# Kernel optimization log

Measured on AMD Instinct MI355X. Metric: run time of the kernel, lower is better.

## Reference

```python
import jax, jax.numpy as jnp
import numpy as np

B, HQ, S, D = 2, 16, 2048, 64   # batch, query heads, seq len, head dim
DV = 2 * D                      # value head dim (differential attention)
LAMBDA_INIT = 0.8
EPS = 1e-5
NEG = -1.0e9


def setup_inputs() -> dict:
    key = jax.random.key(0)
    ks = jax.random.split(key, 8)
    return {
        "q": jax.random.normal(ks[0], (B, HQ, S, D), dtype=jnp.float32),
        "k": jax.random.normal(ks[1], (B, HQ, S, D), dtype=jnp.float32),
        "v": jax.random.normal(ks[2], (B, HQ // 2, S, DV), dtype=jnp.float32),
        "lambda_q1": jax.random.normal(ks[3], (D,), dtype=jnp.float32) * 0.1,
        "lambda_k1": jax.random.normal(ks[4], (D,), dtype=jnp.float32) * 0.1,
        "lambda_q2": jax.random.normal(ks[5], (D,), dtype=jnp.float32) * 0.1,
        "lambda_k2": jax.random.normal(ks[6], (D,), dtype=jnp.float32) * 0.1,
        "gn_weight": jnp.ones((HQ * D,), dtype=jnp.float32),
        "gn_bias": jnp.zeros((HQ * D,), dtype=jnp.float32),
    }


def ghostmax(scores):
    # softmax with an implicit extra zero logit per row
    m = jnp.maximum(jnp.max(scores, axis=-1, keepdims=True), 0.0)
    e = jnp.exp(scores - m)
    return e / (jnp.sum(e, axis=-1, keepdims=True) + jnp.exp(-m))


def group_norm(x, weight, bias, num_groups, eps):
    # x: [B, C, S]; normalize each group over (C/G, S) like nn.GroupNorm
    b, c, s = x.shape
    xg = x.reshape(b, num_groups, (c // num_groups) * s)
    mean = jnp.mean(xg, axis=-1, keepdims=True)
    var = jnp.var(xg, axis=-1, keepdims=True)
    xn = ((xg - mean) * jax.lax.rsqrt(var + eps)).reshape(b, c, s)
    return xn * weight[None, :, None] + bias[None, :, None]


def reference(q, k, v, lambda_q1, lambda_k1, lambda_q2, lambda_k2, gn_weight, gn_bias):
    scale = 1.0 / np.sqrt(D).astype(np.float32)
    scores = jnp.einsum("bhqd,bhkd->bhqk", q, k) * scale
    causal = jnp.triu(jnp.full((S, S), NEG, dtype=scores.dtype), k=1)
    scores = scores + causal[None, None]
    w = ghostmax(scores)                                   # [B, HQ, S, S]
    w = w.reshape(B, HQ // 2, 2, S, S)
    lam1 = jnp.exp(jnp.sum(lambda_q1 * lambda_k1))
    lam2 = jnp.exp(jnp.sum(lambda_q2 * lambda_k2))
    lam = lam1 - lam2 + LAMBDA_INIT
    w = w[:, :, 0] - lam * w[:, :, 1]                      # [B, HQ/2, S, S]
    out = jnp.einsum("bhqk,bhkd->bhqd", w, v)              # [B, HQ/2, S, DV]
    out = out.reshape(B, HQ * D, S)                        # faithful to torch reshape
    out = group_norm(out, gn_weight, gn_bias, num_groups=HQ, eps=EPS)
    return out * (1.0 - LAMBDA_INIT)
```

## Files before the change

kernel.cpp:

```cpp
#include <hip/hip_runtime.h>
#include <hip/hip_bf16.h>

constexpr int B_ = 2, HQ_ = 16, HP_ = 8, S_ = 2048, D_ = 64, DV_ = 128;
constexpr float LAMB0 = 0.8f;
constexpr float EPSV = 1e-5f;

constexpr int TQ = 64, TK = 32;
constexpr int KSTR = 72;
constexpr int VSTR = 40;

typedef __attribute__((ext_vector_type(8))) short bf16x8;
typedef __attribute__((ext_vector_type(4))) float f32x4;
typedef __attribute__((ext_vector_type(8))) float f32x8;

__device__ __forceinline__ unsigned short f2bf(float x) {
  __hip_bfloat16 h = __float2bfloat16(x);
  unsigned short u;
  __builtin_memcpy(&u, &h, 2);
  return u;
}
__device__ __forceinline__ float bf2f(unsigned short h) {
  return __uint_as_float((unsigned)h << 16);
}
__device__ __forceinline__ unsigned pack2(unsigned short a, unsigned short b) {
  return (unsigned)a | ((unsigned)b << 16);
}
__device__ __forceinline__ void split8v(f32x8 x, bf16x8& hi, bf16x8& lo) {
  union { bf16x8 v; unsigned short s[8]; } H, L;
#pragma unroll
  for (int j = 0; j < 8; ++j) {
    unsigned short h = f2bf(x[j]);
    H.s[j] = h;
    L.s[j] = f2bf(x[j] - bf2f(h));
  }
  hi = H.v;
  lo = L.v;
}

__launch_bounds__(512, 4)
__global__ void diffattn_fwd(const float* __restrict__ qg, const float* __restrict__ kg,
                             const float* __restrict__ vg,
                             const float* __restrict__ lq1, const float* __restrict__ lk1,
                             const float* __restrict__ lq2, const float* __restrict__ lk2,
                             float* __restrict__ Obuf, float* __restrict__ stats) {
  __shared__ __align__(16) char smem[38912];
  auto Kl = reinterpret_cast<short(*)[2][TK][KSTR]>(smem);
  auto Vt = reinterpret_cast<short(*)[DV_][VSTR]>(smem + 18432);
  float* mbuf = reinterpret_cast<float*>(smem);
  __shared__ float redbuf[8];

  const int tid = threadIdx.x;
  const int w = tid >> 6;
  const int hw = w >> 2;
  const int qs = w & 3;
  const int l = tid & 63;
  const int g = l >> 4;
  const int li = l & 15;

  const int t = blockIdx.x;
  const int bh = t & 15;
  const int b = bh >> 3;
  const int hp = bh & 7;
  const int u = t >> 4;
  const int qt = (u & 1) ? (31 - (u >> 1)) : (u >> 1);
  const int q0 = qt * TQ;
  const int qw = q0 + qs * 16;

  float d1 = 0.f, d2 = 0.f;
  for (int i = 0; i < D_; ++i) { d1 += lq1[i] * lk1[i]; d2 += lq2[i] * lk2[i]; }
  const float lam = __expf(d1) - __expf(d2) + LAMB0;

  bf16x8 qhi[2], qlo[2];
#pragma unroll
  for (int c = 0; c < 2; ++c) {
    const float* p = qg + (((size_t)b * HQ_ + 2 * hp + hw) * S_ + qw + li) * D_ + c * 32 + g * 8;
    f32x8 x = *reinterpret_cast<const f32x8*>(p);
    split8v(x, qhi[c], qlo[c]);
  }

  float mreg = 0.f;
  float lreg = 1.f;
  const f32x4 zero4 = {0.f, 0.f, 0.f, 0.f};
  f32x4 Oacc[8];
#pragma unroll
  for (int d = 0; d < 8; ++d) Oacc[d] = zero4;

  const int khs = tid >> 8;
  const int kidx = tid & 255;
  const int krow = kidx >> 3;
  const int kcol8 = (kidx & 7) * 8;
  const float* kb0 = kg + ((size_t)b * HQ_ + 2 * hp + khs) * S_ * D_;
  const int vdv = tid & 127;
  const int vk8 = (tid >> 7) * 8;
  const float* vb0 = vg + ((size_t)b * HP_ + hp) * S_ * DV_ + vdv;
  const int vswz = ((vdv >> 3) & 3) << 3;

  const int nkt = (q0 + TQ) / TK;

  for (int kt = 0; kt < nkt; ++kt) {
    const int k0 = kt * TK;
    __syncthreads();

    {
      f32x8 kx = *reinterpret_cast<const f32x8*>(kb0 + (size_t)(k0 + krow) * D_ + kcol8);
      const float* vb = vb0 + (size_t)k0 * DV_;
      f32x8 vx;
#pragma unroll
      for (int j = 0; j < 8; ++j) vx[j] = vb[(size_t)(vk8 + j) * DV_];
      bf16x8 hi, lo;
      split8v(kx, hi, lo);
      *reinterpret_cast<bf16x8*>(&Kl[khs][0][krow][kcol8]) = hi;
      *reinterpret_cast<bf16x8*>(&Kl[khs][1][krow][kcol8]) = lo;
      split8v(vx, hi, lo);
      *reinterpret_cast<bf16x8*>(&Vt[0][vdv][vk8 ^ vswz]) = hi;
      *reinterpret_cast<bf16x8*>(&Vt[1][vdv][vk8 ^ vswz]) = lo;
    }
    __syncthreads();

    if (k0 > qw + 15) continue;
    const bool needmask = (k0 + TK - 1 > qw);
    const int qglob = qw + li;

    bf16x8 kf[2][2][2];
#pragma unroll
    for (int hl = 0; hl < 2; ++hl)
#pragma unroll
      for (int ms = 0; ms < 2; ++ms)
#pragma unroll
        for (int c = 0; c < 2; ++c)
          kf[hl][ms][c] =
              *reinterpret_cast<const bf16x8*>(&Kl[hw][hl][ms * 16 + li][c * 32 + g * 8]);

    f32x4 sT[2] = {zero4, zero4};
    __builtin_amdgcn_s_setprio(1);
#pragma unroll
    for (int ms = 0; ms < 2; ++ms)
#pragma unroll
      for (int c = 0; c < 2; ++c) {
        sT[ms] = __builtin_amdgcn_mfma_f32_16x16x32_bf16(kf[0][ms][c], qhi[c], sT[ms], 0, 0, 0);
        sT[ms] = __builtin_amdgcn_mfma_f32_16x16x32_bf16(kf[0][ms][c], qlo[c], sT[ms], 0, 0, 0);
        sT[ms] = __builtin_amdgcn_mfma_f32_16x16x32_bf16(kf[1][ms][c], qhi[c], sT[ms], 0, 0, 0);
      }
    __builtin_amdgcn_s_setprio(0);

    float sv[2][4];
#pragma unroll
    for (int ms = 0; ms < 2; ++ms)
#pragma unroll
      for (int r = 0; r < 4; ++r) {
        float v = sT[ms][r] * 0.125f;
        if (needmask && (k0 + ms * 16 + g * 4 + r > qglob)) v = -1e30f;
        sv[ms][r] = v;
      }
    float tmax = fmaxf(fmaxf(fmaxf(sv[0][0], sv[0][1]), fmaxf(sv[0][2], sv[0][3])),
                       fmaxf(fmaxf(sv[1][0], sv[1][1]), fmaxf(sv[1][2], sv[1][3])));
    tmax = fmaxf(tmax, __shfl_xor(tmax, 16));
    tmax = fmaxf(tmax, __shfl_xor(tmax, 32));

    if (__any(tmax > mreg + 8.f)) {
      const float mnew = fmaxf(mreg, tmax);
      const float fh = __expf(mreg - mnew);
      mreg = mnew;
      lreg *= fh;
      float fr[4];
#pragma unroll
      for (int r = 0; r < 4; ++r) fr[r] = __shfl(fh, 20 * g + r);
#pragma unroll
      for (int d = 0; d < 8; ++d) {
        f32x4 o = Oacc[d];
        o[0] *= fr[0]; o[1] *= fr[1]; o[2] *= fr[2]; o[3] *= fr[3];
        Oacc[d] = o;
      }
    }

    float p[2][4], psum = 0.f;
#pragma unroll
    for (int ms = 0; ms < 2; ++ms)
#pragma unroll
      for (int r = 0; r < 4; ++r) {
        p[ms][r] = __expf(sv[ms][r] - mreg);
        psum += p[ms][r];
      }
    psum += __shfl_xor(psum, 16);
    psum += __shfl_xor(psum, 32);
    lreg += psum;

    unsigned ph0a = pack2(f2bf(p[0][0]), f2bf(p[0][1]));
    unsigned ph0b = pack2(f2bf(p[0][2]), f2bf(p[0][3]));
    unsigned ph1a = pack2(f2bf(p[1][0]), f2bf(p[1][1]));
    unsigned ph1b = pack2(f2bf(p[1][2]), f2bf(p[1][3]));
    float pl[2][4];
#pragma unroll
    for (int ms = 0; ms < 2; ++ms)
#pragma unroll
      for (int r = 0; r < 4; ++r) pl[ms][r] = p[ms][r] - bf2f(f2bf(p[ms][r]));
    unsigned pl0a = pack2(f2bf(pl[0][0]), f2bf(pl[0][1]));
    unsigned pl0b = pack2(f2bf(pl[0][2]), f2bf(pl[0][3]));
    unsigned pl1a = pack2(f2bf(pl[1][0]), f2bf(pl[1][1]));
    unsigned pl1b = pack2(f2bf(pl[1][2]), f2bf(pl[1][3]));

    const int srcA = 32 * (g & 1) + li;
    const int srcB = srcA + 16;
    const bool hiMs = (g >> 1) != 0;
    bf16x8 AH, AL;
    {
      union { bf16x8 v; unsigned us[4]; } U;
      unsigned a0 = (unsigned)__shfl((int)ph0a, srcA), b0 = (unsigned)__shfl((int)ph1a, srcA);
      unsigned a1 = (unsigned)__shfl((int)ph0b, srcA), b1 = (unsigned)__shfl((int)ph1b, srcA);
      unsigned a2 = (unsigned)__shfl((int)ph0a, srcB), b2 = (unsigned)__shfl((int)ph1a, srcB);
      unsigned a3 = (unsigned)__shfl((int)ph0b, srcB), b3 = (unsigned)__shfl((int)ph1b, srcB);
      U.us[0] = hiMs ? b0 : a0; U.us[1] = hiMs ? b1 : a1;
      U.us[2] = hiMs ? b2 : a2; U.us[3] = hiMs ? b3 : a3;
      AH = U.v;
    }
    {
      union { bf16x8 v; unsigned us[4]; } U;
      unsigned a0 = (unsigned)__shfl((int)pl0a, srcA), b0 = (unsigned)__shfl((int)pl1a, srcA);
      unsigned a1 = (unsigned)__shfl((int)pl0b, srcA), b1 = (unsigned)__shfl((int)pl1b, srcA);
      unsigned a2 = (unsigned)__shfl((int)pl0a, srcB), b2 = (unsigned)__shfl((int)pl1a, srcB);
      unsigned a3 = (unsigned)__shfl((int)pl0b, srcB), b3 = (unsigned)__shfl((int)pl1b, srcB);
      U.us[0] = hiMs ? b0 : a0; U.us[1] = hiMs ? b1 : a1;
      U.us[2] = hiMs ? b2 : a2; U.us[3] = hiMs ? b3 : a3;
      AL = U.v;
    }

    __builtin_amdgcn_s_setprio(1);
#pragma unroll
    for (int dvt = 0; dvt < 8; ++dvt) {
      const int dvr = dvt * 16 + li;
      const int vcol = (g * 8) ^ (((dvr >> 3) & 3) << 3);
      bf16x8 vh = *reinterpret_cast<const bf16x8*>(&Vt[0][dvr][vcol]);
      bf16x8 vl = *reinterpret_cast<const bf16x8*>(&Vt[1][dvr][vcol]);
      f32x4 acc = Oacc[dvt];
      acc = __builtin_amdgcn_mfma_f32_16x16x32_bf16(AH, vh, acc, 0, 0, 0);
      acc = __builtin_amdgcn_mfma_f32_16x16x32_bf16(AL, vh, acc, 0, 0, 0);
      acc = __builtin_amdgcn_mfma_f32_16x16x32_bf16(AH, vl, acc, 0, 0, 0);
      Oacc[dvt] = acc;
    }
    __builtin_amdgcn_s_setprio(0);
  }

  __syncthreads();
  if (w >= 4) {
    float rl[4];
#pragma unroll
    for (int r = 0; r < 4; ++r) rl[r] = lam / __shfl(lreg, 20 * g + r);
#pragma unroll
    for (int dvt = 0; dvt < 8; ++dvt)
#pragma unroll
      for (int r = 0; r < 4; ++r)
        mbuf[((qs * 32 + dvt * 4 + r) * 64) + l] = Oacc[dvt][r] * rl[r];
  }
  __syncthreads();

  float lsum = 0.f, lss = 0.f;
  if (w < 4) {
    float rl[4];
#pragma unroll
    for (int r = 0; r < 4; ++r) rl[r] = 1.f / __shfl(lreg, 20 * g + r);
    float* ob = Obuf + ((size_t)(b * HP_ + hp)) * S_ * DV_;
#pragma unroll
    for (int dvt = 0; dvt < 8; ++dvt)
#pragma unroll
      for (int r = 0; r < 4; ++r) {
        float vres = Oacc[dvt][r] * rl[r] - mbuf[((qs * 32 + dvt * 4 + r) * 64) + l];
        ob[(size_t)(qw + g * 4 + r) * DV_ + dvt * 16 + li] = vres;
        lsum += vres;
        lss += vres * vres;
      }
#pragma unroll
    for (int o = 1; o < 64; o <<= 1) {
      lsum += __shfl_xor(lsum, o);
      lss += __shfl_xor(lss, o);
    }
    if (l == 0) {
      redbuf[w * 2] = lsum;
      redbuf[w * 2 + 1] = lss;
    }
  }
  __syncthreads();
  if (tid == 0) {
    const int region = ((b * HP_ + hp) << 1) | (q0 >= 1024 ? 1 : 0);
    atomicAdd(&stats[2 * region + 0], redbuf[0] + redbuf[2] + redbuf[4] + redbuf[6]);
    atomicAdd(&stats[2 * region + 1], redbuf[1] + redbuf[3] + redbuf[5] + redbuf[7]);
  }
}

__global__ void gn_apply(const float* __restrict__ O, const float* __restrict__ stats,
                         const float* __restrict__ gw, const float* __restrict__ gb,
                         float* __restrict__ out) {
  const size_t f = ((size_t)blockIdx.x * 256 + threadIdx.x) * 4;
  const int g = (int)(f >> 17);
  const int sidx = (int)((f >> 7) & 2047);
  const int hp = (int)((f >> 18) & 7);
  const int c = hp * 128 + (sidx >> 4);
  const float mean = stats[2 * g + 0] * (1.f / 131072.f);
  const float var = stats[2 * g + 1] * (1.f / 131072.f) - mean * mean;
  const float sc = rsqrtf(var + EPSV) * gw[c] * 0.2f;
  const float bi = gb[c] * 0.2f;
  float4 x = *reinterpret_cast<const float4*>(O + f);
  float4 y;
  y.x = (x.x - mean) * sc + bi;
  y.y = (x.y - mean) * sc + bi;
  y.z = (x.z - mean) * sc + bi;
  y.w = (x.w - mean) * sc + bi;
  *reinterpret_cast<float4*>(out + f) = y;
}

extern "C" void kernel_launch(void* const* d_in, const int* in_sizes, int n_in,
                              void* d_out, int out_size, void* d_ws, size_t ws_size,
                              hipStream_t stream) {
  const float* q = (const float*)d_in[0];
  const float* k = (const float*)d_in[1];
  const float* v = (const float*)d_in[2];
  const float* lq1 = (const float*)d_in[3];
  const float* lk1 = (const float*)d_in[4];
  const float* lq2 = (const float*)d_in[5];
  const float* lk2 = (const float*)d_in[6];
  const float* gw = (const float*)d_in[7];
  const float* gb = (const float*)d_in[8];
  float* out = (float*)d_out;

  float* Obuf = (float*)d_ws;
  float* stats = (float*)((char*)d_ws + (size_t)B_ * HP_ * S_ * DV_ * sizeof(float));

  hipMemsetAsync(stats, 0, 64 * sizeof(float), stream);
  diffattn_fwd<<<dim3(512), dim3(512), 0, stream>>>(q, k, v, lq1, lk1, lq2, lk2, Obuf, stats);
  gn_apply<<<dim3(4096), dim3(256), 0, stream>>>(Obuf, stats, gw, gb, out);
}
```

Before: 275.1 us.

## Double-buffer K/V LDS tiles with register prefetch and change LDS strides

New measurement: 813.7 us. 2.96x slower.

```diff
diff --git a/kernel.cpp b/kernel.cpp
--- a/kernel.cpp
+++ b/kernel.cpp
@@ -6,8 +6,8 @@
 constexpr float EPSV = 1e-5f;
 
 constexpr int TQ = 64, TK = 32;
-constexpr int KSTR = 72;
-constexpr int VSTR = 40;
+constexpr int KSTR = 76;
+constexpr int VSTR = 36;
 
 typedef __attribute__((ext_vector_type(8))) short bf16x8;
 typedef __attribute__((ext_vector_type(4))) float f32x4;
@@ -43,9 +43,9 @@
                              const float* __restrict__ lq1, const float* __restrict__ lk1,
                              const float* __restrict__ lq2, const float* __restrict__ lk2,
                              float* __restrict__ Obuf, float* __restrict__ stats) {
-  __shared__ __align__(16) char smem[38912];
-  auto Kl = reinterpret_cast<short(*)[2][TK][KSTR]>(smem);
-  auto Vt = reinterpret_cast<short(*)[DV_][VSTR]>(smem + 18432);
+  __shared__ __align__(16) char smem[75776];
+  auto Kl = reinterpret_cast<short(*)[2][2][TK][KSTR]>(smem);
+  auto Vt = reinterpret_cast<short(*)[2][DV_][VSTR]>(smem + 38912);
   float* mbuf = reinterpret_cast<float*>(smem);
   __shared__ float redbuf[8];
 
@@ -94,26 +94,34 @@
   const int vk8 = (tid >> 7) * 8;
   const float* vb0 = vg + ((size_t)b * HP_ + hp) * S_ * DV_ + vdv;
   const int vswz = ((vdv >> 3) & 3) << 3;
+  const int vcolw = vk8 ^ vswz;
 
   const int nkt = (q0 + TQ) / TK;
+
+  f32x8 kx, vx;
+  kx = *reinterpret_cast<const f32x8*>(kb0 + (size_t)krow * D_ + kcol8);
+#pragma unroll
+  for (int j = 0; j < 8; ++j) vx[j] = vb0[(size_t)(vk8 + j) * DV_];
 
   for (int kt = 0; kt < nkt; ++kt) {
     const int k0 = kt * TK;
-    __syncthreads();
+    const int p_ = kt & 1;
 
     {
-      f32x8 kx = *reinterpret_cast<const f32x8*>(kb0 + (size_t)(k0 + krow) * D_ + kcol8);
-      const float* vb = vb0 + (size_t)k0 * DV_;
-      f32x8 vx;
-#pragma unroll
-      for (int j = 0; j < 8; ++j) vx[j] = vb[(size_t)(vk8 + j) * DV_];
       bf16x8 hi, lo;
       split8v(kx, hi, lo);
-      *reinterpret_cast<bf16x8*>(&Kl[khs][0][krow][kcol8]) = hi;
-      *reinterpret_cast<bf16x8*>(&Kl[khs][1][krow][kcol8]) = lo;
+      *reinterpret_cast<bf16x8*>(&Kl[p_][khs][0][krow][kcol8]) = hi;
+      *reinterpret_cast<bf16x8*>(&Kl[p_][khs][1][krow][kcol8]) = lo;
       split8v(vx, hi, lo);
-      *reinterpret_cast<bf16x8*>(&Vt[0][vdv][vk8 ^ vswz]) = hi;
-      *reinterpret_cast<bf16x8*>(&Vt[1][vdv][vk8 ^ vswz]) = lo;
+      *reinterpret_cast<bf16x8*>(&Vt[p_][0][vdv][vcolw]) = hi;
+      *reinterpret_cast<bf16x8*>(&Vt[p_][1][vdv][vcolw]) = lo;
+    }
+    if (kt + 1 < nkt) {
+      const int kn = (kt + 1) * TK;
+      kx = *reinterpret_cast<const f32x8*>(kb0 + (size_t)(kn + krow) * D_ + kcol8);
+      const float* vb = vb0 + (size_t)kn * DV_;
+#pragma unroll
+      for (int j = 0; j < 8; ++j) vx[j] = vb[(size_t)(vk8 + j) * DV_];
     }
     __syncthreads();
 
@@ -129,7 +137,7 @@
 #pragma unroll
         for (int c = 0; c < 2; ++c)
           kf[hl][ms][c] =
-              *reinterpret_cast<const bf16x8*>(&Kl[hw][hl][ms * 16 + li][c * 32 + g * 8]);
+              *reinterpret_cast<const bf16x8*>(&Kl[p_][hw][hl][ms * 16 + li][c * 32 + g * 8]);
 
     f32x4 sT[2] = {zero4, zero4};
     __builtin_amdgcn_s_setprio(1);
@@ -229,8 +237,8 @@
     for (int dvt = 0; dvt < 8; ++dvt) {
       const int dvr = dvt * 16 + li;
       const int vcol = (g * 8) ^ (((dvr >> 3) & 3) << 3);
-      bf16x8 vh = *reinterpret_cast<const bf16x8*>(&Vt[0][dvr][vcol]);
-      bf16x8 vl = *reinterpret_cast<const bf16x8*>(&Vt[1][dvr][vcol]);
+      bf16x8 vh = *reinterpret_cast<const bf16x8*>(&Vt[p_][0][dvr][vcol]);
+      bf16x8 vl = *reinterpret_cast<const bf16x8*>(&Vt[p_][1][dvr][vcol]);
       f32x4 acc = Oacc[dvt];
       acc = __builtin_amdgcn_mfma_f32_16x16x32_bf16(AH, vh, acc, 0, 0, 0);
       acc = __builtin_amdgcn_mfma_f32_16x16x32_bf16(AL, vh, acc, 0, 0, 0);
```
